# Kernel optimization log

Hardware: AMD Instinct MI355X
Metric: run time of the kernel (lower is better)

Reference implementation:

```python
import jax, jax.numpy as jnp
import numpy as np

G = 16          # grid_size
B = 2           # num graphs
SPACING = 1.5   # anchor_spacing
KA = 8          # atom_k_neighbors
KG = 24         # k_neighbors (grid->atom)
CUTOFF = 8.0
T = 16          # n_atom_types
H = 240         # hidden irreps dim (64x0e+32x1o+16x2e)
A = 9           # SH attr dim, lmax=2
C = 32          # code_dim
L = 2           # num_layers
BIG = 1e9

# real spherical harmonics, 'integral' normalization, e3nn component order
C0 = 0.28209479177387814   # 1/(2 sqrt(pi))
C1 = 0.4886025119029199    # sqrt(3/(4 pi))
C2A = 1.0925484305920792   # sqrt(15/(4 pi))
C2B = 0.31539156525252005  # sqrt(5/(16 pi))
C2C = 0.5462742152960396   # sqrt(15/(16 pi))

def _sph(rel, dist):
    u = rel / jnp.maximum(dist, 1e-9)[:, None]
    x, y, z = u[:, 0], u[:, 1], u[:, 2]
    return jnp.stack([
        jnp.full_like(x, C0),
        C1 * y, C1 * z, C1 * x,
        C2A * x * y, C2A * y * z, C2B * (3.0 * z * z - 1.0),
        C2A * z * x, C2C * (x * x - y * y),
    ], axis=-1)


def setup_inputs():
    key = jax.random.key(0)
    ks = jax.random.split(key, 12)
    Na = 1024
    half = G * SPACING / 2.0
    pos = jax.random.uniform(ks[0], (Na, 3), minval=-half, maxval=half, dtype=jnp.float32)
    atom_types = jax.random.randint(ks[1], (Na,), 0, T, dtype=jnp.int32)
    atom_batch = jnp.repeat(jnp.arange(B, dtype=jnp.int32), Na // B)

    def lin(k, shape):
        fan_in = shape[-2]
        return jax.random.normal(k, shape, dtype=jnp.float32) / jnp.sqrt(float(fan_in))

    Din = 2 * H + A
    return dict(
        pos=pos, atom_types=atom_types, atom_batch=atom_batch,
        We=lin(ks[2], (T + A, H)), be=jnp.zeros((H,), jnp.float32),
        Wm1=lin(ks[3], (L, Din, H)), bm1=jnp.zeros((L, H), jnp.float32),
        Wm2=lin(ks[4], (L, H, H)), bm2=jnp.zeros((L, H), jnp.float32),
        Wu1=lin(ks[5], (L, Din, H)), bu1=jnp.zeros((L, H), jnp.float32),
        Wu2=lin(ks[6], (L, H, H)), bu2=jnp.zeros((L, H), jnp.float32),
        Wo1=lin(ks[7], (H, H)), bo1=jnp.zeros((H,), jnp.float32),
        Wo2=lin(ks[8], (H, C)), bo2=jnp.zeros((C,), jnp.float32),
    )


def _forward(pos, atom_types, atom_batch, We, be, Wm1, bm1, Wm2, bm2,
             Wu1, bu1, Wu2, bu2, Wo1, bo1, Wo2, bo2):
    Na = pos.shape[0]
    ng = G ** 3
    Ng = B * ng
    N = Na + Ng

    # anchor grid, centered, spacing SPACING
    ax = (jnp.arange(G, dtype=pos.dtype) - (G - 1) / 2.0) * SPACING
    grid = jnp.stack(jnp.meshgrid(ax, ax, ax, indexing='ij'), -1).reshape(-1, 3)  # [ng,3]
    grid_flat = jnp.tile(grid, (B, 1))                                            # [Ng,3]
    grid_batch = jnp.repeat(jnp.arange(B, dtype=atom_batch.dtype), ng)
    node_pos = jnp.concatenate([pos, grid_flat], 0)                               # [N,3]

    # atom-atom knn_graph (no self loops, per-graph)
    d2 = jnp.sum((pos[:, None] - pos[None]) ** 2, -1)                             # [Na,Na]
    d2 = jnp.where(atom_batch[:, None] == atom_batch[None], d2, BIG)
    d2 = jnp.where(jnp.eye(Na, dtype=bool), BIG, d2)
    _, nbr = jax.lax.top_k(-d2, KA)                                               # [Na,KA]

    # grid->atom knn (per-graph), edge src=atom, dst=grid node
    d2g = jnp.sum((grid_flat[:, None] - pos[None]) ** 2, -1)                      # [Ng,Na]
    d2g = jnp.where(grid_batch[:, None] == atom_batch[None], d2g, BIG)
    _, nbg = jax.lax.top_k(-d2g, KG)                                              # [Ng,KG]

    src = jnp.concatenate([nbr.reshape(-1), nbg.reshape(-1)])
    dst = jnp.concatenate([jnp.repeat(jnp.arange(Na), KA),
                           Na + jnp.repeat(jnp.arange(Ng), KG)])

    rel = node_pos[src] - node_pos[dst]
    dist = jnp.linalg.norm(rel, axis=-1)
    mask = (dist <= CUTOFF).astype(pos.dtype)        # cutoff as mask (jit-friendly)
    ea = _sph(rel, dist) * mask[:, None]             # [E,A]

    # node attrs: scatter-mean of edge SH over destination nodes
    na_sum = jax.ops.segment_sum(ea, dst, num_segments=N)
    cnt = jax.ops.segment_sum(mask, dst, num_segments=N)
    node_attr = na_sum / jnp.maximum(cnt, 1.0)[:, None]
    node_attr = node_attr.at[:, 0].set(1.0)

    # node features: one-hot atoms, zeros for anchors
    feat = jnp.concatenate([jax.nn.one_hot(atom_types, T, dtype=pos.dtype),
                            jnp.zeros((Ng, T), pos.dtype)], 0)
    h = jax.nn.silu(jnp.concatenate([feat, node_attr], -1) @ We + be)

    # SEGNN-style message passing (attr-conditioned MLPs, masked-sum aggregation)
    for l in range(L):
        mi = jnp.concatenate([h[src], h[dst], ea], -1)                            # [E,2H+A]
        m = jax.nn.silu(jax.nn.silu(mi @ Wm1[l] + bm1[l]) @ Wm2[l] + bm2[l])
        m = m * mask[:, None]
        agg = jax.ops.segment_sum(m, dst, num_segments=N)                         # [N,H]
        ui = jnp.concatenate([h, agg, node_attr], -1)                             # [N,2H+A]
        h = h + jax.nn.silu(jax.nn.silu(ui @ Wu1[l] + bu1[l]) @ Wu2[l] + bu2[l])

    out = jax.nn.silu(h @ Wo1 + bo1) @ Wo2 + bo2                                  # [N,C]
    return out[Na:].reshape(B, ng, C)


def reference(pos, atom_types, atom_batch, We, be, Wm1, bm1, Wm2, bm2,
              Wu1, bu1, Wu2, bu2, Wo1, bo1, Wo2, bo2):
    return _forward(pos, atom_types, atom_batch, We, be, Wm1, bm1, Wm2, bm2,
                    Wu1, bu1, Wu2, bu2, Wo1, bo1, Wo2, bo2)
```

## Files before the change

### kernel.cpp

```cpp
#include <hip/hip_runtime.h>
#include <math.h>

#define NA   1024
#define NGRID 4096
#define NB   2
#define NG   (NB*NGRID)
#define NN   (NA+NG)
#define KAK  8
#define KGK  24
#define EAE  (NA*KAK)
#define EGE  (NG*KGK)
#define ET   (EAE+EGE)
#define HD   240
#define TT   16
#define DIN  489
#define CD   32
#define CUTF 8.0f

typedef __attribute__((ext_vector_type(8))) short short8;
typedef __attribute__((ext_vector_type(4))) short short4v;
typedef __attribute__((ext_vector_type(4))) float f32x4;
typedef __attribute__((ext_vector_type(4))) int i32x4;

__device__ __forceinline__ float silu_f(float x) {
    return x / (1.0f + __expf(-x));
}
__device__ __forceinline__ short f2bf(float x) {
    unsigned u = __float_as_uint(x);
    unsigned r = (u + 0x7FFFu + ((u >> 16) & 1u)) >> 16;
    return (short)r;
}
__device__ __forceinline__ float bf2f(short s) {
    return __uint_as_float(((unsigned)(unsigned short)s) << 16);
}
__device__ __forceinline__ unsigned cvt_pk_bf16(float lo, float hi) {
    unsigned r;
    asm("v_cvt_pk_bf16_f32 %0, %1, %2" : "=v"(r) : "v"(lo), "v"(hi));
    return r;
}

template <int K>
__device__ __forceinline__ void wave_topk(unsigned long long key[8], int lane,
                                          int* __restrict__ outp) {
    unsigned long long lmin = key[0];
#pragma unroll
    for (int s = 1; s < 8; ++s) lmin = key[s] < lmin ? key[s] : lmin;
    int myout = -1;
    for (int t = 0; t < K; ++t) {
        unsigned long long m = lmin;
#pragma unroll
        for (int d = 1; d < 64; d <<= 1) {
            unsigned long long o = __shfl_xor(m, d);
            m = o < m ? o : m;
        }
        if (lane == t) myout = (int)(m & 1023u);
        if (m == lmin) {
#pragma unroll
            for (int s = 0; s < 8; ++s) if (key[s] == m) key[s] = ~0ull;
            lmin = key[0];
#pragma unroll
            for (int s = 1; s < 8; ++s) lmin = key[s] < lmin ? key[s] : lmin;
        }
    }
    if (lane < K) outp[lane] = myout;
}

__global__ __launch_bounds__(256) void knn_kernel(const float* __restrict__ pos,
                                                  int* __restrict__ nbr,
                                                  int* __restrict__ nbg) {
    __shared__ float sx[512], sy[512], sz[512];
    int tid = threadIdx.x;
    bool isAtom = blockIdx.x < (NA / 4);
    int q0 = isAtom ? blockIdx.x * 4 : (blockIdx.x - NA / 4) * 4;
    int pbase;
    if (isAtom) pbase = (q0 >= 512) ? 512 : 0;
    else        pbase = (q0 >= NGRID) ? 512 : 0;
    for (int j = tid; j < 512; j += 256) {
        sx[j] = pos[(pbase + j)*3 + 0];
        sy[j] = pos[(pbase + j)*3 + 1];
        sz[j] = pos[(pbase + j)*3 + 2];
    }
    __syncthreads();
    int lane = tid & 63;
    int qq = q0 + (tid >> 6);
    if (isAtom) {
        int i = qq;
        float px = sx[i - pbase], py = sy[i - pbase], pz = sz[i - pbase];
        unsigned long long key[8];
#pragma unroll
        for (int s = 0; s < 8; ++s) {
            int c = s * 64 + lane;
            int j = pbase + c;
            float dx = px - sx[c], dy = py - sy[c], dz = pz - sz[c];
            float d2 = __fadd_rn(__fadd_rn(__fmul_rn(dx,dx), __fmul_rn(dy,dy)), __fmul_rn(dz,dz));
            key[s] = ((unsigned long long)__float_as_uint(d2) << 10) | (unsigned)j;
            if (j == i) key[s] = ~0ull;
        }
        wave_topk<KAK>(key, lane, &nbr[i*KAK]);
    } else {
        int g = qq;
        int gi = g & (NGRID - 1);
        int ix = gi >> 8, iy = (gi >> 4) & 15, iz = gi & 15;
        float px = ((float)ix - 7.5f) * 1.5f;
        float py = ((float)iy - 7.5f) * 1.5f;
        float pz = ((float)iz - 7.5f) * 1.5f;
        unsigned long long key[8];
#pragma unroll
        for (int s = 0; s < 8; ++s) {
            int c = s * 64 + lane;
            int j = pbase + c;
            float dx = px - sx[c], dy = py - sy[c], dz = pz - sz[c];
            float d2 = __fadd_rn(__fadd_rn(__fmul_rn(dx,dx), __fmul_rn(dy,dy)), __fmul_rn(dz,dz));
            key[s] = ((unsigned long long)__float_as_uint(d2) << 10) | (unsigned)j;
        }
        wave_topk<KGK>(key, lane, &nbg[g*KGK]);
    }
}

__global__ void edge_kernel(const float* __restrict__ pos, const int* __restrict__ nbr,
                            const int* __restrict__ nbg, float4* __restrict__ eaA,
                            float4* __restrict__ eaB, float* __restrict__ eaC,
                            float* __restrict__ emask) {
    int e = blockIdx.x * blockDim.x + threadIdx.x;
    if (e >= ET) return;
    int src; float dpx, dpy, dpz;
    if (e < EAE) {
        int d = e >> 3;
        src = nbr[e];
        dpx = pos[d*3]; dpy = pos[d*3+1]; dpz = pos[d*3+2];
    } else {
        int eg = e - EAE;
        src = nbg[eg];
        int gg = eg / KGK;
        int gi = gg % NGRID;
        int ix = gi >> 8, iy = (gi >> 4) & 15, iz = gi & 15;
        dpx = ((float)ix - 7.5f) * 1.5f;
        dpy = ((float)iy - 7.5f) * 1.5f;
        dpz = ((float)iz - 7.5f) * 1.5f;
    }
    float rx = pos[src*3] - dpx, ry = pos[src*3+1] - dpy, rz = pos[src*3+2] - dpz;
    float dist = sqrtf(rx*rx + ry*ry + rz*rz);
    float mask = (dist <= CUTF) ? 1.0f : 0.0f;
    float inv = 1.0f / fmaxf(dist, 1e-9f);
    float x = rx * inv, y = ry * inv, z = rz * inv;
    float s0 = 0.28209479177387814f;
    float s1 = 0.4886025119029199f * y;
    float s2 = 0.4886025119029199f * z;
    float s3 = 0.4886025119029199f * x;
    float s4 = 1.0925484305920792f * x * y;
    float s5 = 1.0925484305920792f * y * z;
    float s6 = 0.31539156525252005f * (3.0f * z * z - 1.0f);
    float s7 = 1.0925484305920792f * z * x;
    float s8 = 0.5462742152960396f * (x * x - y * y);
    eaA[e] = (float4){s0*mask, s1*mask, s2*mask, s3*mask};
    eaB[e] = (float4){s4*mask, s5*mask, s6*mask, s7*mask};
    eaC[e] = s8 * mask;
    emask[e] = mask;
}

__global__ void node_attr_kernel(const float4* __restrict__ eaA, const float4* __restrict__ eaB,
                                 const float* __restrict__ eaC, const float* __restrict__ emask,
                                 float* __restrict__ attr) {
    int n = blockIdx.x * blockDim.x + threadIdx.x;
    if (n >= NN) return;
    int K, e0;
    if (n < NA) { K = KAK; e0 = n * KAK; }
    else        { K = KGK; e0 = EAE + (n - NA) * KGK; }
    float s[9];
#pragma unroll
    for (int a = 0; a < 9; ++a) s[a] = 0.f;
    float cnt = 0.f;
    for (int k = 0; k < K; ++k) {
        cnt += emask[e0 + k];
        const float4 a0 = eaA[e0 + k];
        const float4 a1 = eaB[e0 + k];
        s[0] += a0.x; s[1] += a0.y; s[2] += a0.z; s[3] += a0.w;
        s[4] += a1.x; s[5] += a1.y; s[6] += a1.z; s[7] += a1.w;
        s[8] += eaC[e0 + k];
    }
    float invc = 1.0f / fmaxf(cnt, 1.0f);
    attr[n*9+0] = 1.0f;
#pragma unroll
    for (int a = 1; a < 9; ++a) attr[n*9+a] = s[a] * invc;
}

__global__ void encoder_kernel(const int* __restrict__ types, const float* __restrict__ attr,
                               const float* __restrict__ We, const float* __restrict__ be,
                               float* __restrict__ h) {
    int idx = blockIdx.x * blockDim.x + threadIdx.x;
    int n = idx / HD, j = idx % HD;
    float acc = be[j];
    if (n < NA) acc += We[types[n] * HD + j];
#pragma unroll
    for (int a = 0; a < 9; ++a) acc += attr[n*9+a] * We[(TT + a) * HD + j];
    h[idx] = silu_f(acc);
}

__global__ void convert_all_kernel(const float* __restrict__ Wm2, const float* __restrict__ Wu1,
                                   const float* __restrict__ Wu2, const float* __restrict__ Wm1,
                                   short* __restrict__ wm2t, short* __restrict__ wu1t,
                                   short* __restrict__ wu2t,
                                   short* __restrict__ wzd_hi, short* __restrict__ wzd_lo,
                                   short* __restrict__ wzs_hi, short* __restrict__ wzs_lo) {
    int idx = blockIdx.x * blockDim.x + threadIdx.x;
    if (idx < 131072) {
        int l = idx >> 16, rem = idx & 65535, col = rem >> 8, k = rem & 255;
        short v = 0;
        if (k < 240 && col < 240) v = f2bf(Wm2[(size_t)l*57600 + k*240 + col]);
        wm2t[idx] = v;
    } else if (idx < 393216) {
        int i = idx - 131072;
        int l = i / 131072, rem = i % 131072, col = rem >> 9, k = rem & 511;
        short v = 0;
        if (k < DIN && col < 240) v = f2bf(Wu1[(size_t)l*DIN*240 + (size_t)k*240 + col]);
        wu1t[i] = v;
    } else if (idx < 524288) {
        int i = idx - 393216;
        int l = i >> 16, rem = i & 65535, col = rem >> 8, k = rem & 255;
        short v = 0;
        if (k < 240 && col < 240) v = f2bf(Wu2[(size_t)l*57600 + k*240 + col]);
        wu2t[i] = v;
    } else if (idx < 655360) {
        int i = idx - 524288;
        int l = i >> 16, rem = i & 65535, col = rem >> 8, k = rem & 255;
        float v = 0.f;
        if (k < 240 && col < 240) v = Wm1[(size_t)l*DIN*HD + (size_t)(240 + k)*HD + col];
        short hh = f2bf(v);
        wzd_hi[i] = hh;
        wzd_lo[i] = f2bf(v - bf2f(hh));
    } else {
        int i = idx - 655360;
        int l = i >> 16, rem = i & 65535, col = rem >> 8, k = rem & 255;
        float v = 0.f;
        if (k < 240 && col < 240) v = Wm1[(size_t)l*DIN*HD + (size_t)k*HD + col];
        short hh = f2bf(v);
        wzs_hi[i] = hh;
        wzs_lo[i] = f2bf(v - bf2f(hh));
    }
}

__global__ __launch_bounds__(256) void node_z_mfma_kernel(
        const float* __restrict__ h,
        const short* __restrict__ wzd_hi, const short* __restrict__ wzd_lo,
        const short* __restrict__ wzs_hi, const short* __restrict__ wzs_lo,
        const float* __restrict__ bm1,
        float* __restrict__ Zs, float* __restrict__ Zd) {
    __shared__ __align__(16) short Ahi[32 * 256];
    __shared__ __align__(16) short Alo[32 * 256];
    int tid = threadIdx.x;
    int n0 = blockIdx.x * 32;

#pragma unroll
    for (int it = 0; it < 4; ++it) {
        int idx = it * 256 + tid;
        int row = idx >> 5, q = idx & 31;
        int j = q * 8;
        short8 ohi = {0,0,0,0,0,0,0,0}, olo = {0,0,0,0,0,0,0,0};
        if (j < 240) {
            const float4 a0 = *(const float4*)(h + (size_t)(n0 + row) * HD + j);
            const float4 a1 = *(const float4*)(h + (size_t)(n0 + row) * HD + j + 4);
            float v[8] = {a0.x, a0.y, a0.z, a0.w, a1.x, a1.y, a1.z, a1.w};
#pragma unroll
            for (int a = 0; a < 8; ++a) {
                short hh = f2bf(v[a]);
                ohi[a] = hh;
                olo[a] = f2bf(v[a] - bf2f(hh));
            }
        }
        int boff = row * 512 + ((q * 16) ^ ((row & 7) << 4));
        *(short8*)((char*)Ahi + boff) = ohi;
        *(short8*)((char*)Alo + boff) = olo;
    }
    __syncthreads();

    int wid = tid >> 6, lane = tid & 63;
    int mw = wid >> 1, nw = wid & 1;
    int lg = lane >> 4, lc = lane & 15;
    int col0 = nw * 128;
    int arow = (mw * 16 + lc) * 256;

    f32x4 acc[8];
#pragma unroll
    for (int nt = 0; nt < 8; ++nt) acc[nt] = (f32x4){0.f, 0.f, 0.f, 0.f};
    __builtin_amdgcn_s_setprio(1);
#pragma unroll
    for (int kc = 0; kc < 8; ++kc) {
        int aoff = arow + ((kc * 32 + lg * 8) ^ ((lc & 7) << 3));
        const short8 ahi = *(const short8*)&Ahi[aoff];
        const short8 alo = *(const short8*)&Alo[aoff];
#pragma unroll
        for (int nt = 0; nt < 8; ++nt) {
            size_t bo = (size_t)(col0 + nt*16 + lc) * 256 + kc*32 + lg*8;
            const short8 bhi = *(const short8*)(wzd_hi + bo);
            const short8 blo = *(const short8*)(wzd_lo + bo);
            acc[nt] = __builtin_amdgcn_mfma_f32_16x16x32_bf16(ahi, bhi, acc[nt], 0, 0, 0);
            acc[nt] = __builtin_amdgcn_mfma_f32_16x16x32_bf16(ahi, blo, acc[nt], 0, 0, 0);
            acc[nt] = __builtin_amdgcn_mfma_f32_16x16x32_bf16(alo, bhi, acc[nt], 0, 0, 0);
        }
    }
    __builtin_amdgcn_s_setprio(0);
#pragma unroll
    for (int nt = 0; nt < 8; ++nt) {
        int ncol = col0 + nt * 16 + lc;
        if (ncol < HD) {
            float bias = bm1[ncol];
            float vals[4] = {acc[nt].x, acc[nt].y, acc[nt].z, acc[nt].w};
#pragma unroll
            for (int r = 0; r < 4; ++r)
                Zd[(size_t)(n0 + mw*16 + lg*4 + r) * HD + ncol] = vals[r] + bias;
        }
    }

    if (n0 < NA) {
#pragma unroll
        for (int nt = 0; nt < 8; ++nt) acc[nt] = (f32x4){0.f, 0.f, 0.f, 0.f};
        __builtin_amdgcn_s_setprio(1);
#pragma unroll
        for (int kc = 0; kc < 8; ++kc) {
            int aoff = arow + ((kc * 32 + lg * 8) ^ ((lc & 7) << 3));
            const short8 ahi = *(const short8*)&Ahi[aoff];
            const short8 alo = *(const short8*)&Alo[aoff];
#pragma unroll
            for (int nt = 0; nt < 8; ++nt) {
                size_t bo = (size_t)(col0 + nt*16 + lc) * 256 + kc*32 + lg*8;
                const short8 bhi = *(const short8*)(wzs_hi + bo);
                const short8 blo = *(const short8*)(wzs_lo + bo);
                acc[nt] = __builtin_amdgcn_mfma_f32_16x16x32_bf16(ahi, bhi, acc[nt], 0, 0, 0);
                acc[nt] = __builtin_amdgcn_mfma_f32_16x16x32_bf16(ahi, blo, acc[nt], 0, 0, 0);
                acc[nt] = __builtin_amdgcn_mfma_f32_16x16x32_bf16(alo, bhi, acc[nt], 0, 0, 0);
            }
        }
        __builtin_amdgcn_s_setprio(0);
#pragma unroll
        for (int nt = 0; nt < 8; ++nt) {
            int ncol = col0 + nt * 16 + lc;
            if (ncol < HD) {
                float vals[4] = {acc[nt].x, acc[nt].y, acc[nt].z, acc[nt].w};
#pragma unroll
                for (int r = 0; r < 4; ++r)
                    Zs[(size_t)(n0 + mw*16 + lg*4 + r) * HD + ncol] = vals[r];
            }
        }
    }
}

__global__ __launch_bounds__(256) void msg_gemm_kernel(
        const float* __restrict__ Zs, const float* __restrict__ Zd,
        const int* __restrict__ nbg,
        const float4* __restrict__ eaA, const float4* __restrict__ eaB,
        const float* __restrict__ eaC,
        const float* __restrict__ emask, const float* __restrict__ Wea,
        const short* __restrict__ wm2t, const float* __restrict__ bm2,
        float* __restrict__ agg) {
    __shared__ __align__(16) short Abuf[48 * 256];
    __shared__ __align__(16) float mkbuf[48];
    int tid = threadIdx.x;
    int blk = blockIdx.x;
    int e0 = blk * 48;

    int q = tid & 31;
    int rh = tid >> 5;
    float4 w0[9], w1[9];
    float4 zdA0, zdA1, zdB0, zdB1;
    int srcs[6];
    if (q < 30) {
        int j = q * 8;
#pragma unroll
        for (int a = 0; a < 9; ++a) {
            w0[a] = *(const float4*)(Wea + a * HD + j);
            w1[a] = *(const float4*)(Wea + a * HD + j + 4);
        }
#pragma unroll
        for (int r8 = 0; r8 < 6; ++r8) srcs[r8] = nbg[e0 + rh + r8 * 8];
        int dn0 = NA + blk * 2;
        zdA0 = *(const float4*)(Zd + (size_t)dn0 * HD + j);
        zdA1 = *(const float4*)(Zd + (size_t)dn0 * HD + j + 4);
        zdB0 = *(const float4*)(Zd + (size_t)(dn0 + 1) * HD + j);
        zdB1 = *(const float4*)(Zd + (size_t)(dn0 + 1) * HD + j + 4);
    }
    if (tid < 48) mkbuf[tid] = emask[EAE + e0 + tid];

#pragma unroll
    for (int r8 = 0; r8 < 6; ++r8) {
        int row = rh + r8 * 8;
        i32x4 oi = (i32x4){0, 0, 0, 0};
        if (q < 30) {
            int j = q * 8;
            int eg = e0 + row;
            int srcn = srcs[r8];
            const float4 zs0 = *(const float4*)(Zs + (size_t)srcn * HD + j);
            const float4 zs1 = *(const float4*)(Zs + (size_t)srcn * HD + j + 4);
            const float4 zd0 = (r8 < 3) ? zdA0 : zdB0;
            const float4 zd1 = (r8 < 3) ? zdA1 : zdB1;
            float s0 = zs0.x + zd0.x, s1 = zs0.y + zd0.y, s2 = zs0.z + zd0.z, s3 = zs0.w + zd0.w;
            float s4 = zs1.x + zd1.x, s5 = zs1.y + zd1.y, s6 = zs1.z + zd1.z, s7 = zs1.w + zd1.w;
            const float4 ea0 = eaA[EAE + eg];
            const float4 ea1 = eaB[EAE + eg];
            const float  ea8 = eaC[EAE + eg];
            float ev[9] = {ea0.x, ea0.y, ea0.z, ea0.w, ea1.x, ea1.y, ea1.z, ea1.w, ea8};
#pragma unroll
            for (int a = 0; a < 9; ++a) {
                float e = ev[a];
                s0 += e * w0[a].x; s1 += e * w0[a].y; s2 += e * w0[a].z; s3 += e * w0[a].w;
                s4 += e * w1[a].x; s5 += e * w1[a].y; s6 += e * w1[a].z; s7 += e * w1[a].w;
            }
            oi[0] = (int)cvt_pk_bf16(silu_f(s0), silu_f(s1));
            oi[1] = (int)cvt_pk_bf16(silu_f(s2), silu_f(s3));
            oi[2] = (int)cvt_pk_bf16(silu_f(s4), silu_f(s5));
            oi[3] = (int)cvt_pk_bf16(silu_f(s6), silu_f(s7));
        }
        *(i32x4*)((char*)Abuf + row * 512 + ((q * 16) ^ ((row & 7) << 4))) = oi;
    }
    __syncthreads();

    int wid = tid >> 6, lane = tid & 63;
    int lg = lane >> 4, lc = lane & 15;
    int col0 = wid * 64;

    f32x4 acc[3][4];
#pragma unroll
    for (int mt = 0; mt < 3; ++mt)
#pragma unroll
        for (int nt = 0; nt < 4; ++nt) acc[mt][nt] = (f32x4){0.f, 0.f, 0.f, 0.f};

    __builtin_amdgcn_s_setprio(1);
#pragma unroll
    for (int kc = 0; kc < 8; ++kc) {
        short8 af[3];
#pragma unroll
        for (int mt = 0; mt < 3; ++mt)
            af[mt] = *(const short8*)&Abuf[(mt*16 + lc) * 256 +
                                           ((kc*32 + lg*8) ^ ((lc & 7) << 3))];
#pragma unroll
        for (int nt = 0; nt < 4; ++nt) {
            const short8 bf = *(const short8*)(wm2t + (size_t)(col0 + nt*16 + lc) * 256 + kc*32 + lg*8);
#pragma unroll
            for (int mt = 0; mt < 3; ++mt)
                acc[mt][nt] = __builtin_amdgcn_mfma_f32_16x16x32_bf16(af[mt], bf, acc[mt][nt], 0, 0, 0);
        }
    }
    __builtin_amdgcn_s_setprio(0);

#pragma unroll
    for (int nt = 0; nt < 4; ++nt) {
        int ncol = col0 + nt * 16 + lc;
        float bias = (ncol < HD) ? bm2[ncol] : 0.f;
        float p[3];
#pragma unroll
        for (int mt = 0; mt < 3; ++mt) {
            const float4 mkv = *(const float4*)&mkbuf[mt*16 + lg*4];
            float t0 = silu_f(acc[mt][nt].x + bias) * mkv.x;
            float t1 = silu_f(acc[mt][nt].y + bias) * mkv.y;
            float t2 = silu_f(acc[mt][nt].z + bias) * mkv.z;
            float t3 = silu_f(acc[mt][nt].w + bias) * mkv.w;
            p[mt] = (t0 + t1) + (t2 + t3);
        }
        float v0 = p[0] + ((lg < 2) ? p[1] : 0.f);
        float v1 = ((lg >= 2) ? p[1] : 0.f) + p[2];
        v0 += __shfl_xor(v0, 16); v0 += __shfl_xor(v0, 32);
        v1 += __shfl_xor(v1, 16); v1 += __shfl_xor(v1, 32);
        if (ncol < HD) {
            int node = NA + blk * 2;
            if (lane < 16)      agg[(size_t)(node + 0) * HD + ncol] = v0;
            else if (lane < 32) agg[(size_t)(node + 1) * HD + ncol] = v1;
        }
    }
}

template <int KE, int NPB>
__global__ __launch_bounds__(192) void msg_mfma_kernel(
        const float* __restrict__ Zs, const float* __restrict__ Zd,
        const int* __restrict__ nbrList,
        const float4* __restrict__ eaA, const float4* __restrict__ eaB,
        const float* __restrict__ eaC,
        const float* __restrict__ emask, const float* __restrict__ Wea,
        const short* __restrict__ wm2t, const float* __restrict__ bm2,
        float* __restrict__ agg, int dstBase, int edgeBase) {
    constexpr int ROWS = KE * NPB;
    constexpr int MT = ROWS / 16;
    __shared__ __align__(16) short Abuf[ROWS * 264];
    __shared__ __align__(16) float mkbuf[ROWS];

    int tid = threadIdx.x;
    int b = blockIdx.x;
    int e0 = edgeBase + b * ROWS;

    if (tid < ROWS) mkbuf[tid] = emask[e0 + tid];
    for (int idx = tid; idx < ROWS * 24; idx += 192) {
        int r = idx / 24;
        Abuf[r * 264 + 240 + (idx % 24)] = 0;
    }
    for (int idx = tid; idx < ROWS * 60; idx += 192) {
        int row = idx / 60;
        int j = (idx % 60) * 4;
        int srcn = nbrList[b * ROWS + row];
        int dstn = dstBase + b * NPB + row / KE;
        const float4 zs = *(const float4*)(Zs + (size_t)srcn * HD + j);
        const float4 zd = *(const float4*)(Zd + (size_t)dstn * HD + j);
        float s0 = zs.x + zd.x, s1 = zs.y + zd.y, s2 = zs.z + zd.z, s3 = zs.w + zd.w;
        const float4 ea0 = eaA[e0 + row];
        const float4 ea1 = eaB[e0 + row];
        const float  ea8 = eaC[e0 + row];
        float ev[9] = {ea0.x, ea0.y, ea0.z, ea0.w, ea1.x, ea1.y, ea1.z, ea1.w, ea8};
#pragma unroll
        for (int a = 0; a < 9; ++a) {
            float e = ev[a];
            const float4 w = *(const float4*)(Wea + a * HD + j);
            s0 += e * w.x; s1 += e * w.y; s2 += e * w.z; s3 += e * w.w;
        }
        short4v o;
        o.x = f2bf(silu_f(s0)); o.y = f2bf(silu_f(s1));
        o.z = f2bf(silu_f(s2)); o.w = f2bf(silu_f(s3));
        *(short4v*)&Abuf[row * 264 + j] = o;
    }
    __syncthreads();

    int w = tid / 64, lane = tid % 64;
    int lg = lane >> 4, lc = lane & 15;
    int wcol0 = w * 80;

    f32x4 acc[MT][5];
#pragma unroll
    for (int mt = 0; mt < MT; ++mt)
#pragma unroll
        for (int nt = 0; nt < 5; ++nt) acc[mt][nt] = (f32x4){0.f, 0.f, 0.f, 0.f};

#pragma unroll
    for (int kc = 0; kc < 8; ++kc) {
        short8 af[MT];
#pragma unroll
        for (int mt = 0; mt < MT; ++mt)
            af[mt] = *(const short8*)&Abuf[(mt * 16 + lc) * 264 + kc * 32 + lg * 8];
#pragma unroll
        for (int nt = 0; nt < 5; ++nt) {
            const short8 bf = *(const short8*)(wm2t + (size_t)(wcol0 + nt * 16 + lc) * 256 + kc * 32 + lg * 8);
#pragma unroll
            for (int mt = 0; mt < MT; ++mt)
                acc[mt][nt] = __builtin_amdgcn_mfma_f32_16x16x32_bf16(af[mt], bf, acc[mt][nt], 0, 0, 0);
        }
    }

#pragma unroll
    for (int nt = 0; nt < 5; ++nt) {
        int ncol = wcol0 + nt * 16 + lc;
        float bias = bm2[ncol];
        float p[MT];
#pragma unroll
        for (int mt = 0; mt < MT; ++mt) {
            const float4 mkv = *(const float4*)&mkbuf[mt * 16 + lg * 4];
            float t0 = silu_f(acc[mt][nt].x + bias) * mkv.x;
            float t1 = silu_f(acc[mt][nt].y + bias) * mkv.y;
            float t2 = silu_f(acc[mt][nt].z + bias) * mkv.z;
            float t3 = silu_f(acc[mt][nt].w + bias) * mkv.w;
            p[mt] = (t0 + t1) + (t2 + t3);
        }
#pragma unroll
        for (int mt = 0; mt < MT; ++mt) {
            float v = p[mt];
            v += __shfl_xor(v, 16);
            if (lane < 16)
                agg[(size_t)(dstBase + b * (2 * MT) + 2 * mt + 0) * HD + ncol] = v;
            else if (lane >= 32 && lane < 48)
                agg[(size_t)(dstBase + b * (2 * MT) + 2 * mt + 1) * HD + ncol] = v;
        }
    }
}

__global__ __launch_bounds__(256) void update_mfma_kernel(
        float* __restrict__ h, const float* __restrict__ agg,
        const float* __restrict__ attr,
        const short* __restrict__ wu1t, const float* __restrict__ bu1,
        const short* __restrict__ wu2t, const float* __restrict__ bu2) {
    __shared__ __align__(16) short Abuf[32 * 512];
    __shared__ __align__(16) short Ubuf[32 * 256];
    int tid = threadIdx.x;
    int n0 = blockIdx.x * 32;

#pragma unroll
    for (int it = 0; it < 8; ++it) {
        int idx = it * 256 + tid;
        int row = idx >> 6, q = idx & 63;
        int j = q * 8;
        int n = n0 + row;
        short8 o = {0,0,0,0,0,0,0,0};
        if (j < 240) {
            const float4 a0 = *(const float4*)(h + (size_t)n * HD + j);
            const float4 a1 = *(const float4*)(h + (size_t)n * HD + j + 4);
            o[0]=f2bf(a0.x); o[1]=f2bf(a0.y); o[2]=f2bf(a0.z); o[3]=f2bf(a0.w);
            o[4]=f2bf(a1.x); o[5]=f2bf(a1.y); o[6]=f2bf(a1.z); o[7]=f2bf(a1.w);
        } else if (j < 480) {
            const float4 a0 = *(const float4*)(agg + (size_t)n * HD + (j - 240));
            const float4 a1 = *(const float4*)(agg + (size_t)n * HD + (j - 240) + 4);
            o[0]=f2bf(a0.x); o[1]=f2bf(a0.y); o[2]=f2bf(a0.z); o[3]=f2bf(a0.w);
            o[4]=f2bf(a1.x); o[5]=f2bf(a1.y); o[6]=f2bf(a1.z); o[7]=f2bf(a1.w);
        } else if (j == 480) {
#pragma unroll
            for (int a = 0; a < 8; ++a) o[a] = f2bf(attr[n*9 + a]);
        } else if (j == 488) {
            o[0] = f2bf(attr[n*9 + 8]);
        }
        *(short8*)((char*)Abuf + row * 1024 + ((q * 16) ^ ((row & 7) << 4))) = o;
    }
    __syncthreads();

    int wid = tid >> 6, lane = tid & 63;
    int mw = wid >> 1, nw = wid & 1;
    int lg = lane >> 4, lc = lane & 15;
    int col0 = nw * 128;

    f32x4 acc[8];
#pragma unroll
    for (int nt = 0; nt < 8; ++nt) acc[nt] = (f32x4){0.f, 0.f, 0.f, 0.f};
    __builtin_amdgcn_s_setprio(1);
#pragma unroll
    for (int kc = 0; kc < 16; ++kc) {
        const short8 af = *(const short8*)((char*)Abuf + (mw*16 + lc) * 1024 +
                                           ((kc*64 + lg*16) ^ ((lc & 7) << 4)));
#pragma unroll
        for (int nt = 0; nt < 8; ++nt) {
            const short8 bf = *(const short8*)(wu1t + (size_t)(col0 + nt*16 + lc) * 512 + kc*32 + lg*8);
            acc[nt] = __builtin_amdgcn_mfma_f32_16x16x32_bf16(af, bf, acc[nt], 0, 0, 0);
        }
    }
    __builtin_amdgcn_s_setprio(0);
#pragma unroll
    for (int nt = 0; nt < 8; ++nt) {
        int ncol = col0 + nt * 16 + lc;
        float bias = (ncol < HD) ? bu1[ncol] : 0.f;
        float vals[4] = {acc[nt].x, acc[nt].y, acc[nt].z, acc[nt].w};
#pragma unroll
        for (int r = 0; r < 4; ++r) {
            int row = mw*16 + lg*4 + r;
            *(short*)((char*)Ubuf + row * 512 + ((ncol * 2) ^ ((row & 7) << 4))) =
                f2bf(silu_f(vals[r] + bias));
        }
    }
    __syncthreads();

    f32x4 acc2[8];
#pragma unroll
    for (int nt = 0; nt < 8; ++nt) acc2[nt] = (f32x4){0.f, 0.f, 0.f, 0.f};
    __builtin_amdgcn_s_setprio(1);
#pragma unroll
    for (int kc = 0; kc < 8; ++kc) {
        const short8 af = *(const short8*)((char*)Ubuf + (mw*16 + lc) * 512 +
                                           ((kc*64 + lg*16) ^ ((lc & 7) << 4)));
#pragma unroll
        for (int nt = 0; nt < 8; ++nt) {
            const short8 bf = *(const short8*)(wu2t + (size_t)(col0 + nt*16 + lc) * 256 + kc*32 + lg*8);
            acc2[nt] = __builtin_amdgcn_mfma_f32_16x16x32_bf16(af, bf, acc2[nt], 0, 0, 0);
        }
    }
    __builtin_amdgcn_s_setprio(0);
#pragma unroll
    for (int nt = 0; nt < 8; ++nt) {
        int ncol = col0 + nt * 16 + lc;
        if (ncol < HD) {
            float bias = bu2[ncol];
            float vals[4] = {acc2[nt].x, acc2[nt].y, acc2[nt].z, acc2[nt].w};
#pragma unroll
            for (int r = 0; r < 4; ++r) {
                int row = mw*16 + lg*4 + r;
                size_t hi = (size_t)(n0 + row) * HD + ncol;
                h[hi] += silu_f(vals[r] + bias);
            }
        }
    }
}

__global__ void output_kernel(const float* __restrict__ h,
                              const float* __restrict__ Wo1, const float* __restrict__ bo1,
                              const float* __restrict__ Wo2, const float* __restrict__ bo2,
                              float* __restrict__ out) {
    const int NBT = 4;
    __shared__ float hr[NBT][HD];
    __shared__ float o1[NBT][HD];
    int tid = threadIdx.x;
    int g0 = blockIdx.x * NBT;
    for (int idx = tid; idx < NBT * HD; idx += 256) {
        int k = idx / HD, i = idx % HD;
        hr[k][i] = h[(size_t)(NA + g0 + k) * HD + i];
    }
    __syncthreads();
    int j = tid;
    if (j < HD) {
        float acc[NBT] = {0.f, 0.f, 0.f, 0.f};
        for (int i4 = 0; i4 < 60; ++i4) {
            int i = 4 * i4;
            float w0 = Wo1[(i+0)*HD+j], w1 = Wo1[(i+1)*HD+j];
            float w2 = Wo1[(i+2)*HD+j], w3 = Wo1[(i+3)*HD+j];
#pragma unroll
            for (int k = 0; k < NBT; ++k) {
                const float4 a = *reinterpret_cast<const float4*>(&hr[k][i]);
                acc[k] += a.x*w0 + a.y*w1 + a.z*w2 + a.w*w3;
            }
        }
        float bb = bo1[j];
#pragma unroll
        for (int k = 0; k < NBT; ++k) o1[k][j] = silu_f(acc[k] + bb);
    }
    __syncthreads();
    if (tid < NBT * CD) {
        int k = tid >> 5, c = tid & 31;
        float acc = bo2[c];
        for (int i = 0; i < HD; ++i) acc += o1[k][i] * Wo2[i*CD + c];
        out[(size_t)(g0 + k) * CD + c] = acc;
    }
}

extern "C" void kernel_launch(void* const* d_in, const int* in_sizes, int n_in,
                              void* d_out, int out_size, void* d_ws, size_t ws_size,
                              hipStream_t stream) {
    (void)in_sizes; (void)n_in; (void)out_size; (void)ws_size;
    const float* pos   = (const float*)d_in[0];
    const int*   types = (const int*)d_in[1];
    const int*   batch = (const int*)d_in[2];
    (void)batch;
    const float* We    = (const float*)d_in[3];
    const float* be    = (const float*)d_in[4];
    const float* Wm1   = (const float*)d_in[5];
    const float* bm1   = (const float*)d_in[6];
    const float* Wm2   = (const float*)d_in[7];
    const float* bm2   = (const float*)d_in[8];
    const float* Wu1   = (const float*)d_in[9];
    const float* bu1   = (const float*)d_in[10];
    const float* Wu2   = (const float*)d_in[11];
    const float* bu2   = (const float*)d_in[12];
    const float* Wo1   = (const float*)d_in[13];
    const float* bo1   = (const float*)d_in[14];
    const float* Wo2   = (const float*)d_in[15];
    const float* bo2   = (const float*)d_in[16];
    float* out = (float*)d_out;

    char* ws = (char*)d_ws;
    size_t off = 0;
    auto take = [&](size_t bytes) -> char* {
        char* p = ws + off;
        off = (off + bytes + 255) & ~(size_t)255;
        return p;
    };
    int*    nbr    = (int*)take((size_t)EAE * 4);
    int*    nbg    = (int*)take((size_t)EGE * 4);
    float4* eaA    = (float4*)take((size_t)ET * 16);
    float4* eaB    = (float4*)take((size_t)ET * 16);
    float*  eaC    = (float*)take((size_t)ET * 4);
    float*  emask  = (float*)take((size_t)ET * 4);
    float*  attr   = (float*)take((size_t)NN * 9 * 4);
    float*  h      = (float*)take((size_t)NN * HD * 4);
    float*  agg    = (float*)take((size_t)NN * HD * 4);
    float*  zs     = (float*)take((size_t)NA * HD * 4);
    float*  zd     = (float*)take((size_t)NN * HD * 4);
    short*  wm2t   = (short*)take((size_t)2 * 256 * 256 * 2);
    short*  wu1t   = (short*)take((size_t)2 * 256 * 512 * 2);
    short*  wu2t   = (short*)take((size_t)2 * 256 * 256 * 2);
    short*  wzd_hi = (short*)take((size_t)2 * 256 * 256 * 2);
    short*  wzd_lo = (short*)take((size_t)2 * 256 * 256 * 2);
    short*  wzs_hi = (short*)take((size_t)2 * 256 * 256 * 2);
    short*  wzs_lo = (short*)take((size_t)2 * 256 * 256 * 2);

    knn_kernel<<<NA/4 + NG/4, 256, 0, stream>>>(pos, nbr, nbg);
    edge_kernel<<<ET/256, 256, 0, stream>>>(pos, nbr, nbg, eaA, eaB, eaC, emask);
    node_attr_kernel<<<NN/256, 256, 0, stream>>>(eaA, eaB, eaC, emask, attr);
    encoder_kernel<<<(NN*HD)/256, 256, 0, stream>>>(types, attr, We, be, h);
    convert_all_kernel<<<786432/256, 256, 0, stream>>>(Wm2, Wu1, Wu2, Wm1,
                                                       wm2t, wu1t, wu2t,
                                                       wzd_hi, wzd_lo, wzs_hi, wzs_lo);

    for (int l = 0; l < 2; ++l) {
        const float* wm1 = Wm1 + (size_t)l * DIN * HD;
        const float* wea = wm1 + (size_t)480 * HD;
        const short* w2t = wm2t + (size_t)l * 256 * 256;
        const float* bb2 = bm2 + l * HD;
        node_z_mfma_kernel<<<NN/32, 256, 0, stream>>>(
            h,
            wzd_hi + (size_t)l * 65536, wzd_lo + (size_t)l * 65536,
            wzs_hi + (size_t)l * 65536, wzs_lo + (size_t)l * 65536,
            bm1 + l * HD, zs, zd);
        msg_mfma_kernel<KAK, 8><<<NA*KAK/64, 192, 0, stream>>>(
            zs, zd, nbr, eaA, eaB, eaC, emask, wea, w2t, bb2, agg, 0, 0);
        msg_gemm_kernel<<<EGE/48, 256, 0, stream>>>(zs, zd, nbg, eaA, eaB, eaC,
                                                    emask, wea, w2t, bb2, agg);
        update_mfma_kernel<<<NN/32, 256, 0, stream>>>(
            h, agg, attr,
            wu1t + (size_t)l * 256 * 512, bu1 + l * HD,
            wu2t + (size_t)l * 256 * 256, bu2 + l * HD);
    }
    output_kernel<<<NG/4, 256, 0, stream>>>(h, Wo1, bo1, Wo2, bo2, out);
}
```

Baseline: 622.2 us.

## Fuse encoder and node-Z projection into encoder and update kernels

Removes the standalone encoder and node_z kernels. The encoder now computes h and writes its hi/lo bf16 split straight to LDS, then runs the Z projection in the same block. The layer-0 update kernel writes the new h into LDS and computes the next layer's Z before exiting. This saves two launches per forward pass and the global re-reads of h, at the cost of longer kernels and possible races if the LDS reuse in the update kernel is not synchronised correctly.

```diff
diff --git a/kernel.cpp b/kernel.cpp
--- a/kernel.cpp
+++ b/kernel.cpp
@@ -182,18 +182,6 @@
     attr[n*9+0] = 1.0f;
 #pragma unroll
     for (int a = 1; a < 9; ++a) attr[n*9+a] = s[a] * invc;
-}
-
-__global__ void encoder_kernel(const int* __restrict__ types, const float* __restrict__ attr,
-                               const float* __restrict__ We, const float* __restrict__ be,
-                               float* __restrict__ h) {
-    int idx = blockIdx.x * blockDim.x + threadIdx.x;
-    int n = idx / HD, j = idx % HD;
-    float acc = be[j];
-    if (n < NA) acc += We[types[n] * HD + j];
-#pragma unroll
-    for (int a = 0; a < 9; ++a) acc += attr[n*9+a] * We[(TT + a) * HD + j];
-    h[idx] = silu_f(acc);
 }
 
 __global__ void convert_all_kernel(const float* __restrict__ Wm2, const float* __restrict__ Wu1,
@@ -239,40 +227,12 @@
     }
 }
 
-__global__ __launch_bounds__(256) void node_z_mfma_kernel(
-        const float* __restrict__ h,
+__device__ __forceinline__ void z_mfma_body(
+        const short* __restrict__ Ahi, const short* __restrict__ Alo,
         const short* __restrict__ wzd_hi, const short* __restrict__ wzd_lo,
         const short* __restrict__ wzs_hi, const short* __restrict__ wzs_lo,
-        const float* __restrict__ bm1,
-        float* __restrict__ Zs, float* __restrict__ Zd) {
-    __shared__ __align__(16) short Ahi[32 * 256];
-    __shared__ __align__(16) short Alo[32 * 256];
-    int tid = threadIdx.x;
-    int n0 = blockIdx.x * 32;
-
-#pragma unroll
-    for (int it = 0; it < 4; ++it) {
-        int idx = it * 256 + tid;
-        int row = idx >> 5, q = idx & 31;
-        int j = q * 8;
-        short8 ohi = {0,0,0,0,0,0,0,0}, olo = {0,0,0,0,0,0,0,0};
-        if (j < 240) {
-            const float4 a0 = *(const float4*)(h + (size_t)(n0 + row) * HD + j);
-            const float4 a1 = *(const float4*)(h + (size_t)(n0 + row) * HD + j + 4);
-            float v[8] = {a0.x, a0.y, a0.z, a0.w, a1.x, a1.y, a1.z, a1.w};
-#pragma unroll
-            for (int a = 0; a < 8; ++a) {
-                short hh = f2bf(v[a]);
-                ohi[a] = hh;
-                olo[a] = f2bf(v[a] - bf2f(hh));
-            }
-        }
-        int boff = row * 512 + ((q * 16) ^ ((row & 7) << 4));
-        *(short8*)((char*)Ahi + boff) = ohi;
-        *(short8*)((char*)Alo + boff) = olo;
-    }
-    __syncthreads();
-
+        const float* __restrict__ bm1, float* __restrict__ Zs, float* __restrict__ Zd,
+        int n0, int tid) {
     int wid = tid >> 6, lane = tid & 63;
     int mw = wid >> 1, nw = wid & 1;
     int lg = lane >> 4, lc = lane & 15;
@@ -342,6 +302,56 @@
             }
         }
     }
+}
+
+__global__ __launch_bounds__(256) void encoder_z_kernel(
+        const int* __restrict__ types, const float* __restrict__ attr,
+        const float* __restrict__ We, const float* __restrict__ be,
+        const short* __restrict__ wzd_hi, const short* __restrict__ wzd_lo,
+        const short* __restrict__ wzs_hi, const short* __restrict__ wzs_lo,
+        const float* __restrict__ bm1,
+        float* __restrict__ h, float* __restrict__ Zs, float* __restrict__ Zd) {
+    __shared__ __align__(16) short Ahi[32 * 256];
+    __shared__ __align__(16) short Alo[32 * 256];
+    __shared__ float sattr[32 * 9];
+    int tid = threadIdx.x;
+    int n0 = blockIdx.x * 32;
+    for (int i = tid; i < 288; i += 256) sattr[i] = attr[n0 * 9 + i];
+    __syncthreads();
+
+#pragma unroll
+    for (int it = 0; it < 4; ++it) {
+        int idx = it * 256 + tid;
+        int row = idx >> 5, q = idx & 31;
+        int j = q * 8;
+        int n = n0 + row;
+        short8 ohi = {0,0,0,0,0,0,0,0}, olo = {0,0,0,0,0,0,0,0};
+        if (j < 240) {
+            int tpe = (n < NA) ? types[n] : -1;
+            float4 hv0, hv1;
+            float* hvp[8] = {&hv0.x, &hv0.y, &hv0.z, &hv0.w, &hv1.x, &hv1.y, &hv1.z, &hv1.w};
+#pragma unroll
+            for (int c = 0; c < 8; ++c) {
+                int col = j + c;
+                float acc = be[col];
+                if (tpe >= 0) acc += We[tpe * HD + col];
+#pragma unroll
+                for (int a = 0; a < 9; ++a) acc += sattr[row * 9 + a] * We[(TT + a) * HD + col];
+                float v = silu_f(acc);
+                *hvp[c] = v;
+                short hh = f2bf(v);
+                ohi[c] = hh;
+                olo[c] = f2bf(v - bf2f(hh));
+            }
+            *(float4*)(h + (size_t)n * HD + j) = hv0;
+            *(float4*)(h + (size_t)n * HD + j + 4) = hv1;
+        }
+        int boff = row * 512 + ((q * 16) ^ ((row & 7) << 4));
+        *(short8*)((char*)Ahi + boff) = ohi;
+        *(short8*)((char*)Alo + boff) = olo;
+    }
+    __syncthreads();
+    z_mfma_body(Ahi, Alo, wzd_hi, wzd_lo, wzs_hi, wzs_lo, bm1, Zs, Zd, n0, tid);
 }
 
 __global__ __launch_bounds__(256) void msg_gemm_kernel(
@@ -566,13 +576,20 @@
     }
 }
 
-__global__ __launch_bounds__(256) void update_mfma_kernel(
+template <bool DO_Z>
+__global__ __launch_bounds__(256) void update_z_kernel(
         float* __restrict__ h, const float* __restrict__ agg,
         const float* __restrict__ attr,
         const short* __restrict__ wu1t, const float* __restrict__ bu1,
-        const short* __restrict__ wu2t, const float* __restrict__ bu2) {
+        const short* __restrict__ wu2t, const float* __restrict__ bu2,
+        const short* __restrict__ wzd_hi, const short* __restrict__ wzd_lo,
+        const short* __restrict__ wzs_hi, const short* __restrict__ wzs_lo,
+        const float* __restrict__ bm1,
+        float* __restrict__ Zs, float* __restrict__ Zd) {
     __shared__ __align__(16) short Abuf[32 * 512];
     __shared__ __align__(16) short Ubuf[32 * 256];
+    short* Ahi = Abuf;
+    short* Alo = Abuf + 32 * 256;
     int tid = threadIdx.x;
     int n0 = blockIdx.x * 32;
 
@@ -655,17 +672,30 @@
 #pragma unroll
     for (int nt = 0; nt < 8; ++nt) {
         int ncol = col0 + nt * 16 + lc;
-        if (ncol < HD) {
-            float bias = bu2[ncol];
-            float vals[4] = {acc2[nt].x, acc2[nt].y, acc2[nt].z, acc2[nt].w};
-#pragma unroll
-            for (int r = 0; r < 4; ++r) {
-                int row = mw*16 + lg*4 + r;
-                size_t hi = (size_t)(n0 + row) * HD + ncol;
-                h[hi] += silu_f(vals[r] + bias);
+        float bias = (ncol < HD) ? bu2[ncol] : 0.f;
+        float vals[4] = {acc2[nt].x, acc2[nt].y, acc2[nt].z, acc2[nt].w};
+#pragma unroll
+        for (int r = 0; r < 4; ++r) {
+            int row = mw*16 + lg*4 + r;
+            int zoff = row * 512 + ((ncol * 2) ^ ((row & 7) << 4));
+            if (ncol < HD) {
+                size_t hidx = (size_t)(n0 + row) * HD + ncol;
+                float nh = h[hidx] + silu_f(vals[r] + bias);
+                h[hidx] = nh;
+                if (DO_Z) {
+                    short hh = f2bf(nh);
+                    *(short*)((char*)Ahi + zoff) = hh;
+                    *(short*)((char*)Alo + zoff) = f2bf(nh - bf2f(hh));
+                }
+            } else if (DO_Z) {
+                *(short*)((char*)Ahi + zoff) = 0;
+                *(short*)((char*)Alo + zoff) = 0;
             }
         }
     }
+    if (!DO_Z) return;
+    __syncthreads();
+    z_mfma_body(Ahi, Alo, wzd_hi, wzd_lo, wzs_hi, wzs_lo, bm1, Zs, Zd, n0, tid);
 }
 
 __global__ void output_kernel(const float* __restrict__ h,
@@ -761,29 +791,35 @@
     knn_kernel<<<NA/4 + NG/4, 256, 0, stream>>>(pos, nbr, nbg);
     edge_kernel<<<ET/256, 256, 0, stream>>>(pos, nbr, nbg, eaA, eaB, eaC, emask);
     node_attr_kernel<<<NN/256, 256, 0, stream>>>(eaA, eaB, eaC, emask, attr);
-    encoder_kernel<<<(NN*HD)/256, 256, 0, stream>>>(types, attr, We, be, h);
     convert_all_kernel<<<786432/256, 256, 0, stream>>>(Wm2, Wu1, Wu2, Wm1,
                                                        wm2t, wu1t, wu2t,
                                                        wzd_hi, wzd_lo, wzs_hi, wzs_lo);
+    encoder_z_kernel<<<NN/32, 256, 0, stream>>>(types, attr, We, be,
+                                                wzd_hi, wzd_lo, wzs_hi, wzs_lo,
+                                                bm1, h, zs, zd);
 
     for (int l = 0; l < 2; ++l) {
         const float* wm1 = Wm1 + (size_t)l * DIN * HD;
         const float* wea = wm1 + (size_t)480 * HD;
         const short* w2t = wm2t + (size_t)l * 256 * 256;
         const float* bb2 = bm2 + l * HD;
-        node_z_mfma_kernel<<<NN/32, 256, 0, stream>>>(
-            h,
-            wzd_hi + (size_t)l * 65536, wzd_lo + (size_t)l * 65536,
-            wzs_hi + (size_t)l * 65536, wzs_lo + (size_t)l * 65536,
-            bm1 + l * HD, zs, zd);
         msg_mfma_kernel<KAK, 8><<<NA*KAK/64, 192, 0, stream>>>(
             zs, zd, nbr, eaA, eaB, eaC, emask, wea, w2t, bb2, agg, 0, 0);
         msg_gemm_kernel<<<EGE/48, 256, 0, stream>>>(zs, zd, nbg, eaA, eaB, eaC,
                                                     emask, wea, w2t, bb2, agg);
-        update_mfma_kernel<<<NN/32, 256, 0, stream>>>(
-            h, agg, attr,
-            wu1t + (size_t)l * 256 * 512, bu1 + l * HD,
-            wu2t + (size_t)l * 256 * 256, bu2 + l * HD);
+        if (l == 0) {
+            update_z_kernel<true><<<NN/32, 256, 0, stream>>>(
+                h, agg, attr,
+                wu1t, bu1, wu2t, bu2,
+                wzd_hi + 65536, wzd_lo + 65536, wzs_hi + 65536, wzs_lo + 65536,
+                bm1 + HD, zs, zd);
+        } else {
+            update_z_kernel<false><<<NN/32, 256, 0, stream>>>(
+                h, agg, attr,
+                wu1t + (size_t)256 * 512, bu1 + HD, wu2t + (size_t)256 * 256, bu2 + HD,
+                wzd_hi, wzd_lo, wzs_hi, wzs_lo,
+                bm1, zs, zd);
+        }
     }
     output_kernel<<<NG/4, 256, 0, stream>>>(h, Wo1, bo1, Wo2, bo2, out);
 }
```

Measured after the change: 669.6 us. 7.6% more time.
